# Optimization experiments

Measured on AMD Instinct MI355X. Metric: run time of the kernel, lower is better.

## Reference

```python
import jax, jax.numpy as jnp
import numpy as np

D_K = 64
NEG_INF = -1.0e9


def setup_inputs() -> dict:
    key = jax.random.key(0)
    kq, kk, kv, km = jax.random.split(key, 4)
    B, H, S, D = 4, 16, 2048, D_K
    q = jax.random.normal(kq, (B, H, S, D), dtype=jnp.float32)
    k = jax.random.normal(kk, (B, H, S, D), dtype=jnp.float32)
    v = jax.random.normal(kv, (B, H, S, D), dtype=jnp.float32)
    attn_mask = jax.random.randint(km, (B, H, S, S), 0, 2).astype(jnp.bool_)
    return {"q": q, "k": k, "v": v, "attn_mask": attn_mask}


def reference(q, k, v, attn_mask):
    # scores: [B,H,S,S] = q @ k^T / sqrt(d_k)
    scale = 1.0 / jnp.sqrt(jnp.float32(D_K)).astype(q.dtype)
    attn_score = jnp.einsum("bhqd,bhkd->bhqk", q, k) * scale
    attn_score = jnp.where(attn_mask, jnp.asarray(NEG_INF, attn_score.dtype), attn_score)
    attn_weights = jax.nn.softmax(attn_score, axis=-1)
    # dropout p=0.0 -> identity (deterministic reference)
    output = jnp.einsum("bhqk,bhkd->bhqd", attn_weights, v)
    return (output, attn_weights)
```

## Files before the change

kernel.cpp:

```cpp
#include <hip/hip_runtime.h>
#include <hip/hip_bf16.h>

#define S_LEN 2048
#define DK    64
#define NT64  32
#define O_ELEMS (4 * 16 * 2048 * 64)

typedef float f32x4  __attribute__((ext_vector_type(4)));
typedef short bf16x8 __attribute__((ext_vector_type(8)));

static __device__ __forceinline__ unsigned short f2bf(float f) {
  unsigned int u = __builtin_bit_cast(unsigned int, f);
  u += 0x7fffu + ((u >> 16) & 1u);
  return (unsigned short)(u >> 16);
}

static __device__ __forceinline__ void gload_lds16(const void* g, void* l) {
  __builtin_amdgcn_global_load_lds(
      (const __attribute__((address_space(1))) unsigned int*)g,
      (__attribute__((address_space(3))) unsigned int*)l, 16, 0, 0);
}

__global__ __launch_bounds__(256) void cvt_k_kernel(
    const float* __restrict__ k, unsigned short* __restrict__ k_hi) {
  int i = blockIdx.x * 256 + threadIdx.x;
  float4 v = ((const float4*)k)[i];
  ushort4 h;
  h.x = f2bf(v.x); h.y = f2bf(v.y); h.z = f2bf(v.z); h.w = f2bf(v.w);
  ((ushort4*)k_hi)[i] = h;
}

__global__ __launch_bounds__(256) void transpose_v_kernel(
    const float* __restrict__ v, unsigned short* __restrict__ v_t) {
  __shared__ float tile[64][65];
  const int b  = blockIdx.x;
  const int bh = b >> 5;
  const int j0 = (b & 31) << 6;
  const int t  = threadIdx.x;
  #pragma unroll
  for (int i = 0; i < 4; ++i) {
    int flat = i * 256 + t;
    int jl   = flat >> 4;
    int f4   = flat & 15;
    float4 x = *(const float4*)(v + ((size_t)bh * S_LEN + j0 + jl) * DK + f4 * 4);
    tile[jl][f4 * 4 + 0] = x.x;
    tile[jl][f4 * 4 + 1] = x.y;
    tile[jl][f4 * 4 + 2] = x.z;
    tile[jl][f4 * 4 + 3] = x.w;
  }
  __syncthreads();
  #pragma unroll
  for (int i = 0; i < 4; ++i) {
    int flat = i * 256 + t;
    int d    = flat >> 4;
    int jg   = (flat & 15) << 2;
    ushort4 o;
    o.x = f2bf(tile[jg + 0][d]);
    o.y = f2bf(tile[jg + 1][d]);
    o.z = f2bf(tile[jg + 2][d]);
    o.w = f2bf(tile[jg + 3][d]);
    *(ushort4*)(v_t + ((size_t)bh * DK + d) * S_LEN + j0 + jg) = o;
  }
}

__global__ __launch_bounds__(256, 4) void score_sums(
    const float* __restrict__ q,
    const int* __restrict__ mask,
    const unsigned short* __restrict__ k_hi,
    unsigned int* __restrict__ bits,
    float* __restrict__ sums_out) {
  const int blk = blockIdx.x;
  const int id  = ((blk & 7) << 8) | (blk >> 3);
  const int bh  = id >> 5;
  const int q0  = (id & 31) << 6;
  const int tid = threadIdx.x;
  const int w   = tid >> 6;
  const int ln  = tid & 63;
  const int l15 = ln & 15;
  const int lq  = ln >> 4;

  __shared__ __align__(16) unsigned short kh_s[2][64][64];

  const int r8  = ln >> 3, c8 = ln & 7;
  const int swz = c8 ^ r8;
  const size_t kst = ((size_t)bh * S_LEN + 16 * w + r8) * DK + ((size_t)swz << 3);
  auto stage_K = [&](int t, int b) {
    gload_lds16(k_hi + kst + (size_t)t * (64 * DK),          &kh_s[b][16 * w][0]);
    gload_lds16(k_hi + kst + (size_t)t * (64 * DK) + 8 * DK, &kh_s[b][16 * w + 8][0]);
  };

  const float* qp = q + ((size_t)bh * S_LEN + q0 + (w << 4) + l15) * DK + (lq << 3);
  const float4 qa0 = *(const float4*)(qp);
  const float4 qb0 = *(const float4*)(qp + 4);
  const float4 qa1 = *(const float4*)(qp + 32);
  const float4 qb1 = *(const float4*)(qp + 36);

  const size_t rowb = (size_t)bh * S_LEN + q0 + (w << 4) + (lq << 2);
  const int* mptr = mask + rowb * S_LEN + l15;

  bf16x8 qh[2];
  {
    const float sc = 0.125f * 1.4426950408889634f;
    float vv0[8] = {qa0.x, qa0.y, qa0.z, qa0.w, qb0.x, qb0.y, qb0.z, qb0.w};
    float vv1[8] = {qa1.x, qa1.y, qa1.z, qa1.w, qb1.x, qb1.y, qb1.z, qb1.w};
    #pragma unroll
    for (int i = 0; i < 8; ++i) {
      qh[0][i] = (short)f2bf(vv0[i] * sc);
      qh[1][i] = (short)f2bf(vv1[i] * sc);
    }
  }

  auto qk_tile = [&](const unsigned short* kbase, f32x4 (&acc)[4]) {
    #pragma unroll
    for (int s = 0; s < 4; ++s) {
      #pragma unroll
      for (int c = 0; c < 2; ++c) {
        const int off = (s * 16 + l15) * 64 + ((((c << 2) | lq) ^ (l15 & 7)) << 3);
        const bf16x8 bhf = *(const bf16x8*)(kbase + off);
        acc[s] = __builtin_amdgcn_mfma_f32_16x16x32_bf16(qh[c], bhf, acc[s], 0, 0, 0);
      }
    }
  };

  unsigned mA[16], mB[16];
  float sums[4] = {0.f, 0.f, 0.f, 0.f};
  unsigned mwv[4][4];
  #pragma unroll
  for (int r = 0; r < 4; ++r)
    #pragma unroll
    for (int wo = 0; wo < 4; ++wo) mwv[r][wo] = 0u;

#define LOAD_M(T, M)                                                         \
  _Pragma("unroll") for (int r = 0; r < 4; ++r)                              \
    _Pragma("unroll") for (int s = 0; s < 4; ++s)                            \
      M[r * 4 + s] = (unsigned)mptr[(size_t)r * S_LEN + (T) * 64 + s * 16];

  stage_K(0, 0);
  LOAD_M(0, mA)
  __syncthreads();

#define SA_BODY(T, BUF, MC, MN)                                              \
  {                                                                          \
    if ((T) + 1 < NT64) { stage_K((T) + 1, (BUF) ^ 1); LOAD_M((T) + 1, MN) } \
    f32x4 acc[4];                                                            \
    acc[0] = f32x4{0.f, 0.f, 0.f, 0.f}; acc[1] = f32x4{0.f, 0.f, 0.f, 0.f};  \
    acc[2] = f32x4{0.f, 0.f, 0.f, 0.f}; acc[3] = f32x4{0.f, 0.f, 0.f, 0.f};  \
    qk_tile(&kh_s[BUF][0][0], acc);                                          \
    _Pragma("unroll") for (int r = 0; r < 4; ++r) {                          \
      _Pragma("unroll") for (int s = 0; s < 4; ++s) {                        \
        const unsigned mv = MC[r * 4 + s];                                   \
        mwv[r][(T) >> 3] |= (unsigned)(mv != 0) << (4 * ((T) & 7) + s);      \
        sums[r] += mv ? 0.f : __builtin_amdgcn_exp2f(acc[s][r]);             \
      }                                                                      \
    }                                                                        \
    __syncthreads();                                                         \
  }

  SA_BODY(0, 0, mA, mB)
  for (int tt = 0; tt < 15; ++tt) {
    SA_BODY(2 * tt + 1, 1, mB, mA)
    SA_BODY(2 * tt + 2, 0, mA, mB)
  }
  SA_BODY(31, 1, mB, mA)

  #pragma unroll
  for (int r = 0; r < 4; ++r) {
    float x = sums[r];
    x += __shfl_xor(x, 1, 64);
    x += __shfl_xor(x, 2, 64);
    x += __shfl_xor(x, 4, 64);
    x += __shfl_xor(x, 8, 64);
    if (l15 == 0) sums_out[id * 64 + (w << 4) + (lq << 2) + r] = 1.0f / x;
  }
  unsigned int* bb = bits + ((size_t)id * 256 + tid) * 16;
  #pragma unroll
  for (int r = 0; r < 4; ++r)
    *(uint4*)(bb + 4 * r) = make_uint4(mwv[r][0], mwv[r][1], mwv[r][2], mwv[r][3]);
#undef SA_BODY
#undef LOAD_M
}

__global__ __launch_bounds__(256, 4) void attn_pv(
    const float* __restrict__ q,
    const unsigned int* __restrict__ bits,
    const float* __restrict__ sums_in,
    const unsigned short* __restrict__ k_hi,
    const unsigned short* __restrict__ v_t,
    float* __restrict__ out_o,
    float* __restrict__ out_w) {
  const int blk = blockIdx.x;
  const int id  = ((blk & 7) << 8) | (blk >> 3);
  const int bh  = id >> 5;
  const int q0  = (id & 31) << 6;
  const int tid = threadIdx.x;
  const int w   = tid >> 6;
  const int ln  = tid & 63;
  const int l15 = ln & 15;
  const int lq  = ln >> 4;

  __shared__ __align__(16) unsigned short kh_s[2][64][64];
  __shared__ __align__(16) unsigned short vt_s[2][64][64];
  __shared__ __align__(16) unsigned short p_lds[4][16][64];

  const int r8  = ln >> 3, c8 = ln & 7;
  const int swz = c8 ^ r8;
  const size_t kst = ((size_t)bh * S_LEN + 16 * w + r8) * DK + ((size_t)swz << 3);
  const size_t vst = ((size_t)bh * DK + 16 * w + r8) * S_LEN + ((size_t)swz << 3);

  auto stage_K = [&](int t, int b) {
    gload_lds16(k_hi + kst + (size_t)t * (64 * DK),          &kh_s[b][16 * w][0]);
    gload_lds16(k_hi + kst + (size_t)t * (64 * DK) + 8 * DK, &kh_s[b][16 * w + 8][0]);
  };
  auto stage_V = [&](int t, int b) {
    gload_lds16(v_t + vst + (size_t)t * 64,             &vt_s[b][16 * w][0]);
    gload_lds16(v_t + vst + (size_t)t * 64 + 8 * S_LEN, &vt_s[b][16 * w + 8][0]);
  };

  const float* qp = q + ((size_t)bh * S_LEN + q0 + (w << 4) + l15) * DK + (lq << 3);
  const float4 qa0 = *(const float4*)(qp);
  const float4 qb0 = *(const float4*)(qp + 4);
  const float4 qa1 = *(const float4*)(qp + 32);
  const float4 qb1 = *(const float4*)(qp + 36);
  const uint4* bq = (const uint4*)(bits + ((size_t)id * 256 + tid) * 16);
  uint4 mq[4];
  #pragma unroll
  for (int r = 0; r < 4; ++r) mq[r] = bq[r];
  const float* sp = sums_in + id * 64 + (w << 4) + (lq << 2);
  float sums[4] = {sp[0], sp[1], sp[2], sp[3]};

  bf16x8 qh[2];
  {
    const float sc = 0.125f * 1.4426950408889634f;
    float vv0[8] = {qa0.x, qa0.y, qa0.z, qa0.w, qb0.x, qb0.y, qb0.z, qb0.w};
    float vv1[8] = {qa1.x, qa1.y, qa1.z, qa1.w, qb1.x, qb1.y, qb1.z, qb1.w};
    #pragma unroll
    for (int i = 0; i < 8; ++i) {
      qh[0][i] = (short)f2bf(vv0[i] * sc);
      qh[1][i] = (short)f2bf(vv1[i] * sc);
    }
  }

  const size_t rowb = (size_t)bh * S_LEN + q0 + (w << 4) + (lq << 2);
  const size_t mofs = rowb * S_LEN + l15;
  const size_t oofs = rowb * DK + l15;

  auto qk_tile = [&](const unsigned short* kbase, f32x4 (&acc)[4]) {
    #pragma unroll
    for (int s = 0; s < 4; ++s) {
      #pragma unroll
      for (int c = 0; c < 2; ++c) {
        const int off = (s * 16 + l15) * 64 + ((((c << 2) | lq) ^ (l15 & 7)) << 3);
        const bf16x8 bhf = *(const bf16x8*)(kbase + off);
        acc[s] = __builtin_amdgcn_mfma_f32_16x16x32_bf16(qh[c], bhf, acc[s], 0, 0, 0);
      }
    }
  };

  f32x4 oacc[4];
  #pragma unroll
  for (int s = 0; s < 4; ++s) oacc[s] = f32x4{0.f, 0.f, 0.f, 0.f};

  stage_K(0, 0);
  stage_V(0, 0);

#define PB_BODY(T, BUF, WAITN)                                               \
  {                                                                          \
    asm volatile("s_waitcnt vmcnt(" #WAITN ")" ::: "memory");                \
    __builtin_amdgcn_s_barrier();                                            \
    __builtin_amdgcn_sched_barrier(0);                                       \
    if ((T) + 1 < NT64) { stage_K((T) + 1, (BUF) ^ 1);                       \
                          stage_V((T) + 1, (BUF) ^ 1); }                     \
    __builtin_amdgcn_sched_barrier(0);      \
    f32x4 acc[4];                                                            \
    acc[0] = f32x4{0.f, 0.f, 0.f, 0.f}; acc[1] = f32x4{0.f, 0.f, 0.f, 0.f};  \
    acc[2] = f32x4{0.f, 0.f, 0.f, 0.f}; acc[3] = f32x4{0.f, 0.f, 0.f, 0.f};  \
    qk_tile(&kh_s[BUF][0][0], acc);                                          \
    const int wsel = (T) >> 3;                                               \
    const int sh0 = 4 * ((T) & 7);                                           \
    float* wbase = out_w + mofs + (size_t)(T) * 64;                          \
    _Pragma("unroll") for (int r = 0; r < 4; ++r) {                          \
      const unsigned mword = wsel == 0 ? mq[r].x : wsel == 1 ? mq[r].y       \
                           : wsel == 2 ? mq[r].z : mq[r].w;                  \
      const int row = (lq << 2) + r;                                         \
      _Pragma("unroll") for (int s = 0; s < 4; ++s) {                        \
        const int m = (int)((mword >> (sh0 + s)) & 1u);                      \
        const float e = m ? 0.f : __builtin_amdgcn_exp2f(acc[s][r]);         \
        const float wn = e * sums[r];                                        \
        wbase[(size_t)r * S_LEN + s * 16] = wn;                              \
        const int chunk = ((s << 1) | (l15 >> 3)) ^ (row & 7);               \
        p_lds[w][row][(chunk << 3) | (l15 & 7)] = f2bf(wn);                  \
      }                                                                      \
    }                                                                        \
    __builtin_amdgcn_wave_barrier();                                         \
    _Pragma("unroll") for (int c = 0; c < 2; ++c) {                          \
      const bf16x8 pa = *(const bf16x8*)                                     \
          &p_lds[w][l15][((((c << 2) | lq)) ^ (l15 & 7)) << 3];              \
      _Pragma("unroll") for (int s = 0; s < 4; ++s) {                        \
        const int off = (s * 16 + l15) * 64 +                                \
                        ((((c << 2) | lq) ^ (l15 & 7)) << 3);                \
        const bf16x8 vb = *(const bf16x8*)(&vt_s[BUF][0][0] + off);          \
        oacc[s] = __builtin_amdgcn_mfma_f32_16x16x32_bf16(pa, vb, oacc[s],   \
                                                          0, 0, 0);          \
      }                                                                      \
    }                                                                        \
    __builtin_amdgcn_wave_barrier();                                         \
  }

  PB_BODY(0, 0, 0)
  for (int tt = 0; tt < 15; ++tt) {
    PB_BODY(2 * tt + 1, 1, 16)
    PB_BODY(2 * tt + 2, 0, 16)
  }
  PB_BODY(31, 1, 16)

  #pragma unroll
  for (int s = 0; s < 4; ++s) {
    #pragma unroll
    for (int r = 0; r < 4; ++r) {
      out_o[oofs + (size_t)r * DK + s * 16] = oacc[s][r];
    }
  }
#undef PB_BODY
}

extern "C" void kernel_launch(void* const* d_in, const int* in_sizes, int n_in,
                              void* d_out, int out_size, void* d_ws, size_t ws_size,
                              hipStream_t stream) {
  (void)in_sizes; (void)n_in; (void)out_size; (void)ws_size;
  const float* q = (const float*)d_in[0];
  const float* k = (const float*)d_in[1];
  const float* v = (const float*)d_in[2];
  const int* mask = (const int*)d_in[3];

  float* out_o = (float*)d_out;
  float* out_w = out_o + (size_t)O_ELEMS;

  unsigned short* k_hi = (unsigned short*)d_ws;
  unsigned short* v_t  = k_hi + (size_t)O_ELEMS;
  unsigned int*   bits = (unsigned int*)(v_t + (size_t)O_ELEMS);
  float*          sums = (float*)(bits + (size_t)2048 * 256 * 16);

  cvt_k_kernel<<<8192, 256, 0, stream>>>(k, k_hi);
  transpose_v_kernel<<<2048, 256, 0, stream>>>(v, v_t);
  score_sums<<<2048, 256, 0, stream>>>(q, mask, k_hi, bits, sums);
  attn_pv<<<2048, 256, 0, stream>>>(q, bits, sums, k_hi, v_t, out_o, out_w);
}
```

Measured before the change: 589.9 us.

## Load mask with vectorized int4 reads and redistribute bits via LDS

Mask loads in the score pass change from 16 scalar 4-byte gathers per lane (strided by 16 columns) to four contiguous int4 loads per lane. Each lane packs its 16 booleans into a bitmask, writes it to a double-buffered LDS array, and after the barrier reads back the bits matching the MFMA output layout. This aims to cut the number of global load instructions and improve coalescing on the large mask read. In exchange it adds LDS traffic and bit manipulation per tile.

Result: no change. 595.8 us (+1.0%).

```diff
diff --git a/kernel.cpp b/kernel.cpp
--- a/kernel.cpp
+++ b/kernel.cpp
@@ -80,6 +80,7 @@
   const int lq  = ln >> 4;
 
   __shared__ __align__(16) unsigned short kh_s[2][64][64];
+  __shared__ unsigned int pm_lds[2][4][64];
 
   const int r8  = ln >> 3, c8 = ln & 7;
   const int swz = c8 ^ r8;
@@ -95,8 +96,8 @@
   const float4 qa1 = *(const float4*)(qp + 32);
   const float4 qb1 = *(const float4*)(qp + 36);
 
-  const size_t rowb = (size_t)bh * S_LEN + q0 + (w << 4) + (lq << 2);
-  const int* mptr = mask + rowb * S_LEN + l15;
+  const int* mp4 = mask + ((size_t)bh * S_LEN + q0 + 16 * w + (ln >> 2)) * S_LEN
+                        + 4 * (ln & 3);
 
   bf16x8 qh[2];
   {
@@ -122,7 +123,7 @@
     }
   };
 
-  unsigned mA[16], mB[16];
+  int4 mA4[4], mB4[4];
   float sums[4] = {0.f, 0.f, 0.f, 0.f};
   unsigned mwv[4][4];
   #pragma unroll
@@ -130,38 +131,54 @@
     #pragma unroll
     for (int wo = 0; wo < 4; ++wo) mwv[r][wo] = 0u;
 
-#define LOAD_M(T, M)                                                         \
-  _Pragma("unroll") for (int r = 0; r < 4; ++r)                              \
-    _Pragma("unroll") for (int s = 0; s < 4; ++s)                            \
-      M[r * 4 + s] = (unsigned)mptr[(size_t)r * S_LEN + (T) * 64 + s * 16];
+#define LOAD_M4(T, M)                                                        \
+  _Pragma("unroll") for (int j = 0; j < 4; ++j)                              \
+    M[j] = *(const int4*)(mp4 + (size_t)(T) * 64 + 16 * j);
+
+#define PACK_WRITE(M, PBUF)                                                  \
+  {                                                                          \
+    unsigned p = 0;                                                          \
+    _Pragma("unroll") for (int j = 0; j < 4; ++j) {                          \
+      p |= (unsigned)(M[j].x != 0) << (4 * j + 0);                           \
+      p |= (unsigned)(M[j].y != 0) << (4 * j + 1);                           \
+      p |= (unsigned)(M[j].z != 0) << (4 * j + 2);                           \
+      p |= (unsigned)(M[j].w != 0) << (4 * j + 3);                           \
+    }                                                                        \
+    pm_lds[PBUF][w][ln] = p;                                                 \
+  }
 
   stage_K(0, 0);
-  LOAD_M(0, mA)
+  LOAD_M4(0, mA4)
+  PACK_WRITE(mA4, 0)
   __syncthreads();
 
-#define SA_BODY(T, BUF, MC, MN)                                              \
+#define SA_BODY(T, BUF, MN)                                                  \
   {                                                                          \
-    if ((T) + 1 < NT64) { stage_K((T) + 1, (BUF) ^ 1); LOAD_M((T) + 1, MN) } \
+    if ((T) + 1 < NT64) { stage_K((T) + 1, (BUF) ^ 1); LOAD_M4((T) + 1, MN) }\
     f32x4 acc[4];                                                            \
     acc[0] = f32x4{0.f, 0.f, 0.f, 0.f}; acc[1] = f32x4{0.f, 0.f, 0.f, 0.f};  \
     acc[2] = f32x4{0.f, 0.f, 0.f, 0.f}; acc[3] = f32x4{0.f, 0.f, 0.f, 0.f};  \
     qk_tile(&kh_s[BUF][0][0], acc);                                          \
+    unsigned Qr[4];                                                          \
+    _Pragma("unroll") for (int r = 0; r < 4; ++r)                            \
+      Qr[r] = pm_lds[BUF][w][(lq << 4) + (r << 2) + (l15 >> 2)] >> (l15 & 3);\
     _Pragma("unroll") for (int r = 0; r < 4; ++r) {                          \
       _Pragma("unroll") for (int s = 0; s < 4; ++s) {                        \
-        const unsigned mv = MC[r * 4 + s];                                   \
-        mwv[r][(T) >> 3] |= (unsigned)(mv != 0) << (4 * ((T) & 7) + s);      \
-        sums[r] += mv ? 0.f : __builtin_amdgcn_exp2f(acc[s][r]);             \
+        const unsigned m = (Qr[r] >> (4 * s)) & 1u;                          \
+        mwv[r][(T) >> 3] |= m << (4 * ((T) & 7) + s);                        \
+        sums[r] += m ? 0.f : __builtin_amdgcn_exp2f(acc[s][r]);              \
       }                                                                      \
     }                                                                        \
+    if ((T) + 1 < NT64) { PACK_WRITE(MN, (BUF) ^ 1) }                        \
     __syncthreads();                                                         \
   }
 
-  SA_BODY(0, 0, mA, mB)
+  SA_BODY(0, 0, mB4)
   for (int tt = 0; tt < 15; ++tt) {
-    SA_BODY(2 * tt + 1, 1, mB, mA)
-    SA_BODY(2 * tt + 2, 0, mA, mB)
-  }
-  SA_BODY(31, 1, mB, mA)
+    SA_BODY(2 * tt + 1, 1, mA4)
+    SA_BODY(2 * tt + 2, 0, mB4)
+  }
+  SA_BODY(31, 1, mA4)
 
   #pragma unroll
   for (int r = 0; r < 4; ++r) {
@@ -177,7 +194,8 @@
   for (int r = 0; r < 4; ++r)
     *(uint4*)(bb + 4 * r) = make_uint4(mwv[r][0], mwv[r][1], mwv[r][2], mwv[r][3]);
 #undef SA_BODY
-#undef LOAD_M
+#undef LOAD_M4
+#undef PACK_WRITE
 }
 
 __global__ __launch_bounds__(256, 4) void attn_pv(
```
